# Kernel tuning notes

Hardware: AMD Instinct MI355X
Metric: run time of the kernel (lower is better)

Reference implementation:

```python
import jax, jax.numpy as jnp
import numpy as np

MARGIN = 0.3
EPS = 1e-12  # matches F.normalize eps


def setup_inputs() -> dict:
    key = jax.random.key(0)
    prompts = jax.random.normal(key, (4096, 2048), dtype=jnp.float32)
    return {"prompts": prompts}


def reference(prompts):
    # L2-normalize rows (F.normalize(dim=1))
    norm = jnp.linalg.norm(prompts, axis=1, keepdims=True)
    p = prompts / jnp.maximum(norm, EPS)
    # pairwise cosine similarity [K, K]
    sim = p @ p.T
    K = sim.shape[0]
    # strict upper triangle (i < j) and strict threshold s > margin
    upper = jnp.triu(jnp.ones((K, K), dtype=bool), k=1)
    viol = upper & (sim > MARGIN)
    count = jnp.sum(viol)
    loss_sum = jnp.sum(jnp.where(viol, sim - MARGIN, jnp.zeros_like(sim)))
    # if no violating pair, loss is 0
    return jnp.where(count == 0,
                     jnp.asarray(0.0, dtype=sim.dtype),
                     loss_sum / jnp.maximum(count, 1).astype(sim.dtype))
```

## Files before the change

kernel.cpp:

```cpp
#include <hip/hip_runtime.h>
#include <stdint.h>

#define MARGIN 0.3f
#define NROWS 4096
#define DIM   2048
#define ROWB  1024
#define BT    128
#define BKB   128
#define NKS   (ROWB / BKB)
#define NB    (NROWS / BT)
#define NBLK  (NB * (NB + 1) / 2)

typedef float f32x4 __attribute__((ext_vector_type(4)));
typedef int   i32x4 __attribute__((ext_vector_type(4)));
typedef int   i32x8 __attribute__((ext_vector_type(8)));
typedef short s16x8 __attribute__((ext_vector_type(8)));

__device__ __forceinline__ ushort f32_to_bf16(float f) {
  uint32_t u = __float_as_uint(f);
  return (ushort)((u + 0x7FFFu + ((u >> 16) & 1u)) >> 16);
}

__device__ __forceinline__ unsigned f32_to_fp4(float y) {
  unsigned s = (__float_as_uint(y) >> 31) << 3;
  float a = fabsf(y);
  unsigned c;
  if      (a < 0.25f) c = 0;
  else if (a < 0.75f) c = 1;
  else if (a < 1.25f) c = 2;
  else if (a < 1.75f) c = 3;
  else if (a < 2.5f)  c = 4;
  else if (a < 3.5f)  c = 5;
  else if (a < 5.0f)  c = 6;
  else                c = 7;
  return s | c;
}

__device__ __forceinline__ void async_load16(const void* g, void* l) {
  __builtin_amdgcn_global_load_lds(
      (const __attribute__((address_space(1))) uint32_t*)g,
      (__attribute__((address_space(3))) uint32_t*)l, 16, 0, 0);
}

template <int FLY>
__global__ __launch_bounds__(256) void prep_kernel(const float* __restrict__ in,
                                                   unsigned char* __restrict__ pn,
                                                   float* __restrict__ invn,
                                                   float* __restrict__ accum) {
  const int row = blockIdx.x;
  const int tid = threadIdx.x;
  if (row == 0 && tid == 0) { accum[0] = 0.f; accum[1] = 0.f; }

  const float4* rp = (const float4*)(in + (size_t)row * DIM);
  float4 v0 = rp[tid * 2];
  float4 v1 = rp[tid * 2 + 1];
  float ss = v0.x*v0.x + v0.y*v0.y + v0.z*v0.z + v0.w*v0.w
           + v1.x*v1.x + v1.y*v1.y + v1.z*v1.z + v1.w*v1.w;
  #pragma unroll
  for (int off = 32; off; off >>= 1) ss += __shfl_down(ss, off);

  __shared__ float wred[4];
  __shared__ float stot;
  const int lane = tid & 63, w = tid >> 6;
  if (lane == 0) wred[w] = ss;
  __syncthreads();
  if (tid == 0) stot = wred[0] + wred[1] + wred[2] + wred[3];
  __syncthreads();
  const float inv = 1.0f / fmaxf(sqrtf(stot), 1e-12f);

  if (FLY) {
    if (tid == 0) invn[row] = inv;
  } else {
    const float sc = inv * 64.0f;
    float e[8] = {v0.x, v0.y, v0.z, v0.w, v1.x, v1.y, v1.z, v1.w};
    uint32_t u = 0;
    #pragma unroll
    for (int j = 0; j < 4; ++j) {
      unsigned lo = f32_to_fp4(e[2*j]   * sc);
      unsigned hi = f32_to_fp4(e[2*j+1] * sc);
      u |= (lo | (hi << 4)) << (8 * j);
    }
    *(uint32_t*)(pn + (size_t)row * ROWB + tid * 4) = u;
  }
}

__global__ __launch_bounds__(256) void tri_gemm(const unsigned char* __restrict__ pn,
                                                float* __restrict__ accum) {
  const int b = blockIdx.x;
  int t = (b & 7) * (NBLK / 8) + (b >> 3);
  int bi = 0;
  while (t >= NB - bi) { t -= NB - bi; ++bi; }
  const int bj = bi + t;

  __shared__ __align__(16) unsigned char Asm[BT * BKB];
  __shared__ __align__(16) unsigned char Bsm[BT * BKB];

  const int tid  = threadIdx.x;
  const int lane = tid & 63;
  const int w    = tid >> 6;
  const int wr   = w >> 1;
  const int wc   = w & 1;

  f32x4 acc[4][4] = {};
  const int rowA = bi * BT, rowB = bj * BT;

  const int srow  = (lane >> 3);
  const int gslot = (lane & 7) ^ srow;

  const unsigned char* gA = pn + (size_t)(rowA + srow) * ROWB + gslot * 16;
  const unsigned char* gB = pn + (size_t)(rowB + srow) * ROWB + gslot * 16;

  const int fr = lane & 15, g = lane >> 4;
  const i32x4 z4 = {0, 0, 0, 0};

  for (int ks = 0; ks < NKS; ++ks) {
    const int kb = ks * BKB;
    if (ks) __syncthreads();
    #pragma unroll
    for (int q = 0; q < 4; ++q) {
      const int r = w * 32 + q * 8;
      async_load16(gA + (size_t)r * ROWB + kb, Asm + r * BKB);
      async_load16(gB + (size_t)r * ROWB + kb, Bsm + r * BKB);
    }
    __syncthreads();

    #pragma unroll
    for (int kk = 0; kk < 2; ++kk) {
      i32x8 af[4], bf[4];
      #pragma unroll
      for (int m = 0; m < 4; ++m) {
        const int ra = wr * 64 + m * 16 + fr;
        i32x4 va = *(const i32x4*)(Asm + ra * BKB + (((kk * 4 + g) ^ (ra & 7)) * 16));
        af[m] = __builtin_shufflevector(va, z4, 0, 1, 2, 3, 4, 5, 6, 7);
        const int rb = wc * 64 + m * 16 + fr;
        i32x4 vb = *(const i32x4*)(Bsm + rb * BKB + (((kk * 4 + g) ^ (rb & 7)) * 16));
        bf[m] = __builtin_shufflevector(vb, z4, 0, 1, 2, 3, 4, 5, 6, 7);
      }
      #pragma unroll
      for (int m = 0; m < 4; ++m)
        #pragma unroll
        for (int n = 0; n < 4; ++n)
          acc[m][n] = __builtin_amdgcn_mfma_scale_f32_16x16x128_f8f6f4(
              af[m], bf[n], acc[m][n],
              4, 4,
              0, 0x79797979,
              0, 0x79797979);
    }
  }

  float lsum = 0.f, lcnt = 0.f;
  const int gib = rowA + wr * 64;
  const int gjb = rowB + wc * 64;
  #pragma unroll
  for (int m = 0; m < 4; ++m) {
    #pragma unroll
    for (int n = 0; n < 4; ++n) {
      #pragma unroll
      for (int r = 0; r < 4; ++r) {
        int gi = gib + m * 16 + (lane >> 4) * 4 + r;
        int gj = gjb + n * 16 + (lane & 15);
        float s = acc[m][n][r];
        if (gi < gj && s > MARGIN) { lsum += s - MARGIN; lcnt += 1.f; }
      }
    }
  }
  #pragma unroll
  for (int off = 32; off; off >>= 1) {
    lsum += __shfl_down(lsum, off);
    lcnt += __shfl_down(lcnt, off);
  }
  __shared__ float rs[4], rc[4];
  if (lane == 0) { rs[w] = lsum; rc[w] = lcnt; }
  __syncthreads();
  if (tid == 0) {
    atomicAdd(&accum[0], rs[0] + rs[1] + rs[2] + rs[3]);
    atomicAdd(&accum[1], rc[0] + rc[1] + rc[2] + rc[3]);
  }
}

__global__ __launch_bounds__(256) void tri_gemm_fly(const float* __restrict__ inF,
                                                    const float* __restrict__ invn,
                                                    float* __restrict__ accum) {
  enum { FBK = 64 };
  int t = blockIdx.x, bi = 0;
  while (t >= NB - bi) { t -= NB - bi; ++bi; }
  const int bj = bi + t;

  __shared__ __align__(16) ushort Asm[BT * FBK];
  __shared__ __align__(16) ushort Bsm[BT * FBK];

  const int tid  = threadIdx.x;
  const int lane = tid & 63;
  const int w    = tid >> 6;
  const int wr   = w >> 1, wc = w & 1;

  f32x4 acc[4][4] = {};
  const int rowA = bi * BT, rowB = bj * BT;

  for (int k0 = 0; k0 < DIM; k0 += FBK) {
    if (k0) __syncthreads();
    #pragma unroll
    for (int p = 0; p < 8; ++p) {
      int c   = p * 256 + tid;
      int isB = c >> 10;
      int cc  = c & 1023;
      int r   = cc >> 3;
      int s   = cc & 7;
      const int grow = (isB ? rowB : rowA) + r;
      const float4* src = (const float4*)(inF + (size_t)grow * DIM + k0 + s * 8);
      float4 v0 = src[0], v1 = src[1];
      int4 pack;
      ushort* h = (ushort*)&pack;
      h[0] = f32_to_bf16(v0.x); h[1] = f32_to_bf16(v0.y);
      h[2] = f32_to_bf16(v0.z); h[3] = f32_to_bf16(v0.w);
      h[4] = f32_to_bf16(v1.x); h[5] = f32_to_bf16(v1.y);
      h[6] = f32_to_bf16(v1.z); h[7] = f32_to_bf16(v1.w);
      *(int4*)((isB ? Bsm : Asm) + r * FBK + (s ^ (r & 7)) * 8) = pack;
    }
    __syncthreads();

    s16x8 af[2][4], bfv[2][4];
    const int fr = lane & 15, hi = lane >> 4;
    #pragma unroll
    for (int kk = 0; kk < 2; ++kk)
      #pragma unroll
      for (int m = 0; m < 4; ++m) {
        const int ra = wr * 64 + m * 16 + fr;
        af[kk][m] = *(const s16x8*)(Asm + ra * FBK + ((kk * 4 + hi) ^ (ra & 7)) * 8);
        const int rb = wc * 64 + m * 16 + fr;
        bfv[kk][m] = *(const s16x8*)(Bsm + rb * FBK + ((kk * 4 + hi) ^ (rb & 7)) * 8);
      }
    #pragma unroll
    for (int kk = 0; kk < 2; ++kk)
      #pragma unroll
      for (int m = 0; m < 4; ++m)
        #pragma unroll
        for (int n = 0; n < 4; ++n)
          acc[m][n] = __builtin_amdgcn_mfma_f32_16x16x32_bf16(af[kk][m], bfv[kk][n],
                                                              acc[m][n], 0, 0, 0);
  }

  float lsum = 0.f, lcnt = 0.f;
  const int gib = rowA + wr * 64;
  const int gjb = rowB + wc * 64;
  #pragma unroll
  for (int m = 0; m < 4; ++m)
    #pragma unroll
    for (int n = 0; n < 4; ++n)
      #pragma unroll
      for (int r = 0; r < 4; ++r) {
        int gi = gib + m * 16 + (lane >> 4) * 4 + r;
        int gj = gjb + n * 16 + (lane & 15);
        float s = acc[m][n][r] * invn[gi] * invn[gj];
        if (gi < gj && s > MARGIN) { lsum += s - MARGIN; lcnt += 1.f; }
      }
  #pragma unroll
  for (int off = 32; off; off >>= 1) {
    lsum += __shfl_down(lsum, off);
    lcnt += __shfl_down(lcnt, off);
  }
  __shared__ float rs[4], rc[4];
  if (lane == 0) { rs[w] = lsum; rc[w] = lcnt; }
  __syncthreads();
  if (tid == 0) {
    atomicAdd(&accum[0], rs[0] + rs[1] + rs[2] + rs[3]);
    atomicAdd(&accum[1], rc[0] + rc[1] + rc[2] + rc[3]);
  }
}

__global__ void finalize_kernel(const float* __restrict__ accum, float* __restrict__ out) {
  if (threadIdx.x == 0) out[0] = (accum[1] < 0.5f) ? 0.0f : accum[0] / accum[1];
}

extern "C" void kernel_launch(void* const* d_in, const int* in_sizes, int n_in,
                              void* d_out, int out_size, void* d_ws, size_t ws_size,
                              hipStream_t stream) {
  const float* in = (const float*)d_in[0];
  float* out = (float*)d_out;
  const size_t pn_bytes = (size_t)NROWS * ROWB;

  if (ws_size >= pn_bytes + 2 * sizeof(float)) {
    unsigned char* pn = (unsigned char*)d_ws;
    float* accum = (float*)((char*)d_ws + pn_bytes);
    prep_kernel<0><<<NROWS, 256, 0, stream>>>(in, pn, nullptr, accum);
    tri_gemm<<<NBLK, 256, 0, stream>>>(pn, accum);
    finalize_kernel<<<1, 64, 0, stream>>>(accum, out);
  } else {
    float* invn  = (float*)d_ws;
    float* accum = (float*)((char*)d_ws + NROWS * sizeof(float));
    prep_kernel<1><<<NROWS, 256, 0, stream>>>(in, nullptr, invn, accum);
    tri_gemm_fly<<<NBLK, 256, 0, stream>>>(in, invn, accum);
    finalize_kernel<<<1, 64, 0, stream>>>(accum, out);
  }
}
```

Measured before the change: 39.57 us.

## Store fp4 rows in k-plane layout and load MFMA fragments directly from global

The prep kernel now writes packed fp4 data in a plane-major layout: each 16-byte k-chunk of every row is contiguous across rows. The GEMM kernel drops its LDS staging, swizzle and block barriers. Each wave loads its MFMA operand fragments straight from global memory into registers, with a two-stage register double buffer that overlaps loads with MFMAs. This removes the LDS round trip and the synchronisation, but gives up sharing of tiles across waves, so global and L2 traffic rises.

```diff
diff --git a/kernel.cpp b/kernel.cpp
--- a/kernel.cpp
+++ b/kernel.cpp
@@ -5,9 +5,9 @@
 #define NROWS 4096
 #define DIM   2048
 #define ROWB  1024
+#define PLANE (NROWS * 16)
+#define KSTEP (4 * PLANE)
 #define BT    128
-#define BKB   128
-#define NKS   (ROWB / BKB)
 #define NB    (NROWS / BT)
 #define NBLK  (NB * (NB + 1) / 2)
 
@@ -36,12 +36,6 @@
   return s | c;
 }
 
-__device__ __forceinline__ void async_load16(const void* g, void* l) {
-  __builtin_amdgcn_global_load_lds(
-      (const __attribute__((address_space(1))) uint32_t*)g,
-      (__attribute__((address_space(3))) uint32_t*)l, 16, 0, 0);
-}
-
 template <int FLY>
 __global__ __launch_bounds__(256) void prep_kernel(const float* __restrict__ in,
                                                    unsigned char* __restrict__ pn,
@@ -80,7 +74,37 @@
       unsigned hi = f32_to_fp4(e[2*j+1] * sc);
       u |= (lo | (hi << 4)) << (8 * j);
     }
-    *(uint32_t*)(pn + (size_t)row * ROWB + tid * 4) = u;
+    const int plane = tid >> 2;
+    const int sub   = (tid & 3) * 4;
+    *(uint32_t*)(pn + (size_t)plane * PLANE + (size_t)row * 16 + sub) = u;
+  }
+}
+
+__device__ __forceinline__ void ld8(const unsigned char* __restrict__ p,
+                                    uint32_t voA, uint32_t voB,
+                                    i32x4 fa[4], i32x4 fb[4]) {
+  #pragma unroll
+  for (int m = 0; m < 4; ++m) {
+    fa[m] = *(const i32x4*)(p + voA + m * 256);
+    fb[m] = *(const i32x4*)(p + voB + m * 256);
+  }
+}
+
+__device__ __forceinline__ void mm16(const i32x4 fa[4], const i32x4 fb[4],
+                                     f32x4 acc[4][4]) {
+  const i32x4 z4 = {0, 0, 0, 0};
+  #pragma unroll
+  for (int m = 0; m < 4; ++m) {
+    i32x8 am = __builtin_shufflevector(fa[m], z4, 0, 1, 2, 3, 4, 5, 6, 7);
+    #pragma unroll
+    for (int n = 0; n < 4; ++n) {
+      i32x8 bn = __builtin_shufflevector(fb[n], z4, 0, 1, 2, 3, 4, 5, 6, 7);
+      acc[m][n] = __builtin_amdgcn_mfma_scale_f32_16x16x128_f8f6f4(
+          am, bn, acc[m][n],
+          4, 4,
+          0, 0x79797979,
+          0, 0x79797979);
+    }
   }
 }
 
@@ -92,60 +116,35 @@
   while (t >= NB - bi) { t -= NB - bi; ++bi; }
   const int bj = bi + t;
 
-  __shared__ __align__(16) unsigned char Asm[BT * BKB];
-  __shared__ __align__(16) unsigned char Bsm[BT * BKB];
-
   const int tid  = threadIdx.x;
   const int lane = tid & 63;
   const int w    = tid >> 6;
   const int wr   = w >> 1;
   const int wc   = w & 1;
+  const int fr   = lane & 15;
+  const int gq   = lane >> 4;
 
   f32x4 acc[4][4] = {};
   const int rowA = bi * BT, rowB = bj * BT;
 
-  const int srow  = (lane >> 3);
-  const int gslot = (lane & 7) ^ srow;
-
-  const unsigned char* gA = pn + (size_t)(rowA + srow) * ROWB + gslot * 16;
-  const unsigned char* gB = pn + (size_t)(rowB + srow) * ROWB + gslot * 16;
-
-  const int fr = lane & 15, g = lane >> 4;
-  const i32x4 z4 = {0, 0, 0, 0};
-
-  for (int ks = 0; ks < NKS; ++ks) {
-    const int kb = ks * BKB;
-    if (ks) __syncthreads();
-    #pragma unroll
-    for (int q = 0; q < 4; ++q) {
-      const int r = w * 32 + q * 8;
-      async_load16(gA + (size_t)r * ROWB + kb, Asm + r * BKB);
-      async_load16(gB + (size_t)r * ROWB + kb, Bsm + r * BKB);
-    }
-    __syncthreads();
-
-    #pragma unroll
-    for (int kk = 0; kk < 2; ++kk) {
-      i32x8 af[4], bf[4];
-      #pragma unroll
-      for (int m = 0; m < 4; ++m) {
-        const int ra = wr * 64 + m * 16 + fr;
-        i32x4 va = *(const i32x4*)(Asm + ra * BKB + (((kk * 4 + g) ^ (ra & 7)) * 16));
-        af[m] = __builtin_shufflevector(va, z4, 0, 1, 2, 3, 4, 5, 6, 7);
-        const int rb = wc * 64 + m * 16 + fr;
-        i32x4 vb = *(const i32x4*)(Bsm + rb * BKB + (((kk * 4 + g) ^ (rb & 7)) * 16));
-        bf[m] = __builtin_shufflevector(vb, z4, 0, 1, 2, 3, 4, 5, 6, 7);
-      }
-      #pragma unroll
-      for (int m = 0; m < 4; ++m)
-        #pragma unroll
-        for (int n = 0; n < 4; ++n)
-          acc[m][n] = __builtin_amdgcn_mfma_scale_f32_16x16x128_f8f6f4(
-              af[m], bf[n], acc[m][n],
-              4, 4,
-              0, 0x79797979,
-              0, 0x79797979);
-    }
+  uint32_t voA = (uint32_t)gq * PLANE + (uint32_t)(rowA + wr * 64 + fr) * 16;
+  uint32_t voB = (uint32_t)gq * PLANE + (uint32_t)(rowB + wc * 64 + fr) * 16;
+
+  i32x4 fa0[4], fb0[4], fa1[4], fb1[4];
+
+  ld8(pn, voA, voB, fa0, fb0);
+  voA += KSTEP; voB += KSTEP;
+
+  #pragma unroll 1
+  for (int i = 0; i < 8; ++i) {
+    ld8(pn, voA, voB, fa1, fb1);
+    voA += KSTEP; voB += KSTEP;
+    mm16(fa0, fb0, acc);
+    if (i != 7) {
+      ld8(pn, voA, voB, fa0, fb0);
+      voA += KSTEP; voB += KSTEP;
+    }
+    mm16(fa1, fb1, acc);
   }
 
   float lsum = 0.f, lcnt = 0.f;
```

New measurement: 44.88 us. 1.13x slower.
